# Kernel optimization log

Hardware: AMD Instinct MI355X
Metric: run time of the kernel (lower is better)

The kernel has to match this reference:

```python
import jax, jax.numpy as jnp
import numpy as np

V, D, H, B, LA, LC = 50000, 300, 256, 32, 256, 256


def setup_inputs():
    key = jax.random.key(0)
    ks = jax.random.split(key, 20)
    u = lambda k, sh, sc: jax.random.uniform(k, sh, jnp.float32, -sc, sc)
    s = 1.0 / float(np.sqrt(H))
    return {
        "anchor_input": jax.random.randint(ks[0], (B, LA), 0, V),
        "anchor_length": jax.random.randint(ks[1], (B,), 1, LA + 1),
        "candidate_input": jax.random.randint(ks[2], (B, LC), 0, V),
        "candidate_length": jax.random.randint(ks[3], (B,), 1, LC + 1),
        "batch_size": B,
        "emb": jax.random.normal(ks[4], (V, D), jnp.float32) * 0.1,
        "W_ih_a": u(ks[5], (3 * H, D), s),
        "W_hh_a": u(ks[6], (3 * H, H), s),
        "b_ih_a": u(ks[7], (3 * H,), s),
        "b_hh_a": u(ks[8], (3 * H,), s),
        "W_ih_c": u(ks[9], (3 * H, D + H), s),
        "W_hh_c": u(ks[10], (3 * H, H), s),
        "b_ih_c": u(ks[11], (3 * H,), s),
        "b_hh_c": u(ks[12], (3 * H,), s),
        "Wq": u(ks[13], (H, H), s),
        "Wk": u(ks[14], (H, H), s),
        "v_att": u(ks[15], (H,), s),
    }


def _gru_step(x, h, W_ih, W_hh, b_ih, b_hh):
    # torch GRUCell convention (gate order r, z, n)
    gi = x @ W_ih.T + b_ih
    gh = h @ W_hh.T + b_hh
    ir, iz, inn = jnp.split(gi, 3, axis=-1)
    hr, hz, hn = jnp.split(gh, 3, axis=-1)
    r = jax.nn.sigmoid(ir + hr)
    z = jax.nn.sigmoid(iz + hz)
    n = jnp.tanh(inn + r * hn)
    return (1.0 - z) * n + z * h


def _forward(anchor_input, anchor_length, candidate_input, candidate_length,
             emb, W_ih_a, W_hh_a, b_ih_a, b_hh_a,
             W_ih_c, W_hh_c, b_ih_c, b_hh_c, Wq, Wk, v_att):
    Bb = anchor_input.shape[0]
    # ---- anchor encoder: GRU with packed-sequence semantics (zero pad outputs, freeze hidden) ----
    ax = emb[anchor_input].transpose(1, 0, 2)  # [LA, B, D]
    ts_a = jnp.arange(ax.shape[0])

    def a_step(h, inp):
        xt, t = inp
        hn = _gru_step(xt, h, W_ih_a, W_hh_a, b_ih_a, b_hh_a)
        valid = (t < anchor_length)[:, None]
        h = jnp.where(valid, hn, h)
        return h, jnp.where(valid, hn, 0.0)

    h0 = jnp.zeros((Bb, H), ax.dtype)
    anchor_hidden, a_outs = jax.lax.scan(a_step, h0, (ax, ts_a))  # a_outs: [LA, B, H]
    anchor_outputs = a_outs.transpose(1, 0, 2)  # [B, LA, H]
    anchor_emb = a_outs.sum(0) / anchor_length.astype(ax.dtype)[:, None]  # meanVector

    # ---- candidate decoder: per-step additive attention + GRU + length-mask blend ----
    keys = anchor_outputs @ Wk  # [B, LA, H], precomputed once
    cx = emb[candidate_input].transpose(1, 0, 2)  # [LC, B, D]
    ts_c = jnp.arange(cx.shape[0])

    def c_step(h, inp):
        xt, t = inp
        q = h @ Wq  # [B, H] query from previous hidden
        scores = jnp.einsum('blh,h->bl', jnp.tanh(keys + q[:, None, :]), v_att)
        attn = jax.nn.softmax(scores, axis=-1)
        context = jnp.einsum('bl,blh->bh', attn, anchor_outputs)
        hn = _gru_step(jnp.concatenate([xt, context], axis=-1), h,
                       W_ih_c, W_hh_c, b_ih_c, b_hh_c)
        mask = (candidate_length < t).astype(h.dtype)[:, None]  # strict '<' is faithful to source
        h = hn * (1.0 - mask) + mask * h
        return h, h * (1.0 - mask)

    _, c_outs = jax.lax.scan(c_step, anchor_hidden, (cx, ts_c))  # [LC, B, H]
    valid_c = (ts_c[:, None] < candidate_length[None, :]).astype(cx.dtype)[:, :, None]
    candidate_emb = (c_outs * valid_c).sum(0) / candidate_length.astype(cx.dtype)[:, None]
    return anchor_emb, candidate_emb


def reference(anchor_input, anchor_length, candidate_input, candidate_length, batch_size,
              emb, W_ih_a, W_hh_a, b_ih_a, b_hh_a,
              W_ih_c, W_hh_c, b_ih_c, b_hh_c, Wq, Wk, v_att):
    return _forward(anchor_input, anchor_length, candidate_input, candidate_length,
                    emb, W_ih_a, W_hh_a, b_ih_a, b_hh_a,
                    W_ih_c, W_hh_c, b_ih_c, b_hh_c, Wq, Wk, v_att)
```

## Files before the change

### kernel.cpp

```cpp
#include <hip/hip_runtime.h>
#include <hip/hip_fp16.h>
#include <math.h>

#define BB 32
#define LAV 256
#define LCV 256
#define DV 300
#define HV 256
#define G3 768

typedef _Float16 f16x2 __attribute__((ext_vector_type(2)));
union F4H8 { float4 f4; f16x2 h2[4]; };
union U2H4 { uint2 u2; f16x2 h2[2]; };

static __device__ __forceinline__ float rcp_(float x) { return __builtin_amdgcn_rcpf(x); }
static __device__ __forceinline__ float sigm(float x) { return rcp_(1.f + __expf(-x)); }
static __device__ __forceinline__ float tanh_(float x) { return 1.f - 2.f * rcp_(1.f + __expf(2.f * x)); }

__global__ void prep_pack(const float* __restrict__ W_ih_a, const float* __restrict__ W_ih_c,
                          const float* __restrict__ W_hh_a, const float* __restrict__ W_hh_c,
                          const float* __restrict__ Wq,
                          float* __restrict__ WT_a, float* __restrict__ WT_cx,
                          __half* __restrict__ WhaRH, __half* __restrict__ WhaSH,
                          __half* __restrict__ WqH, __half* __restrict__ WrzH,
                          __half* __restrict__ WnH)
{
    int i = blockIdx.x * 256 + threadIdx.x;
    switch (blockIdx.y) {
    case 0: if (i < 230400) { int k = i / 768, n = i % 768; WT_a[i] = W_ih_a[n * 300 + k]; } break;
    case 1: if (i < 230400) { int k = i / 768, n = i % 768; WT_cx[i] = W_ih_c[n * 556 + k]; } break;
    case 2: if (i < 98304) { int e = i & 1, r = i >> 1, ii = r & 63, j = r >> 6;
            WhaRH[i] = __float2half(W_hh_a[j * 256 + 2 * ii + e]); } break;
    case 3: if (i < 98304) { int e = i & 1, s = (i >> 1) & 1, r = i >> 2, j = r % 768, i2 = r / 768;
            int k = 2 * (64 + 2 * i2 + s) + e;
            WhaSH[i] = __float2half(W_hh_a[j * 256 + k]); } break;
    case 4: if (i < 65536) { int e = i & 1, r2 = i >> 1, m = r2 & 255, k2 = r2 >> 8;
            WqH[i] = __float2half(Wq[(2 * k2 + e) * 256 + m]); } break;
    case 5: if (i < 262144) { int e = i & 1, r2 = i >> 1, j = r2 & 511, kk = r2 >> 9;
            int kh = kk >> 7, k2i = kk & 127, k = kh * 256 + 2 * k2i + e;
            float v = (k < 256) ? W_hh_c[j * 256 + k] : W_ih_c[j * 556 + 300 + (k - 256)];
            WrzH[i] = __float2half(v); } break;
    case 6: if (i < 131072) { int e = i & 1, r2 = i >> 1, j = r2 & 255, gg = r2 >> 8;
            int slot = gg >> 6, k2i = gg & 63, grp = slot >> 1, kh = slot & 1;
            int kl = kh * 128 + 2 * k2i + e;
            float v = grp ? W_ih_c[(512 + j) * 556 + 300 + kl] : W_hh_c[(512 + j) * 256 + kl];
            WnH[i] = __float2half(v); } break;
    }
}

template <int MODE>
__global__ __launch_bounds__(256) void gemm_tile(
    const float* __restrict__ X, const int* __restrict__ gidx, int ldx,
    const float* __restrict__ Wt, int K, int Nn,
    const float* __restrict__ bias, float* __restrict__ Cout)
{
    __shared__ __align__(16) float As[32][68];
    __shared__ __align__(16) float Bs[32][68];
    __shared__ int toks[64];
    int tid = threadIdx.x;
    int m0 = blockIdx.x * 64, n0 = blockIdx.y * 64;
    if (tid < 64) {
        int m = m0 + tid;
        if (gidx) { int t = m >> 5, b = m & 31; toks[tid] = gidx[b * LAV + t]; }
        else toks[tid] = m;
    }
    __syncthreads();
    float acc[4][4] = {};
    int tx = tid & 15, ty = tid >> 4;
    for (int k0 = 0; k0 < K; k0 += 32) {
        {
            int r = tid >> 2, cc = (tid & 3) * 8;
            const float* src = X + (size_t)toks[r] * ldx + k0 + cc;
            float4 v0 = {0.f,0.f,0.f,0.f}, v1 = {0.f,0.f,0.f,0.f};
            if (k0 + cc + 3 < K) v0 = *(const float4*)src;
            if (k0 + cc + 7 < K) v1 = *(const float4*)(src + 4);
            As[cc+0][r]=v0.x; As[cc+1][r]=v0.y; As[cc+2][r]=v0.z; As[cc+3][r]=v0.w;
            As[cc+4][r]=v1.x; As[cc+5][r]=v1.y; As[cc+6][r]=v1.z; As[cc+7][r]=v1.w;
        }
        {
            int kr = tid >> 4, c4 = (tid & 15) * 4;
            #pragma unroll
            for (int p = 0; p < 2; ++p) {
                float4 v = {0.f,0.f,0.f,0.f};
                int kg = k0 + kr + p * 16;
                if (kg < K) v = *(const float4*)(Wt + (size_t)kg * Nn + n0 + c4);
                *(float4*)&Bs[kr + p * 16][c4] = v;
            }
        }
        __syncthreads();
        #pragma unroll 8
        for (int kk = 0; kk < 32; ++kk) {
            float4 a4 = *(const float4*)&As[kk][ty * 4];
            float4 b4 = *(const float4*)&Bs[kk][tx * 4];
            acc[0][0]=fmaf(a4.x,b4.x,acc[0][0]); acc[0][1]=fmaf(a4.x,b4.y,acc[0][1]);
            acc[0][2]=fmaf(a4.x,b4.z,acc[0][2]); acc[0][3]=fmaf(a4.x,b4.w,acc[0][3]);
            acc[1][0]=fmaf(a4.y,b4.x,acc[1][0]); acc[1][1]=fmaf(a4.y,b4.y,acc[1][1]);
            acc[1][2]=fmaf(a4.y,b4.z,acc[1][2]); acc[1][3]=fmaf(a4.y,b4.w,acc[1][3]);
            acc[2][0]=fmaf(a4.z,b4.x,acc[2][0]); acc[2][1]=fmaf(a4.z,b4.y,acc[2][1]);
            acc[2][2]=fmaf(a4.z,b4.z,acc[2][2]); acc[2][3]=fmaf(a4.z,b4.w,acc[2][3]);
            acc[3][0]=fmaf(a4.w,b4.x,acc[3][0]); acc[3][1]=fmaf(a4.w,b4.y,acc[3][1]);
            acc[3][2]=fmaf(a4.w,b4.z,acc[3][2]); acc[3][3]=fmaf(a4.w,b4.w,acc[3][3]);
        }
        __syncthreads();
    }
    if (MODE == 0) {
        float4 bz = *(const float4*)&bias[n0 + tx * 4];
        #pragma unroll
        for (int i = 0; i < 4; ++i) {
            int m = m0 + ty * 4 + i;
            float4 o = { acc[i][0] + bz.x, acc[i][1] + bz.y, acc[i][2] + bz.z, acc[i][3] + bz.w };
            *(float4*)&Cout[(size_t)m * Nn + n0 + tx * 4] = o;
        }
    } else {
        int b_ = m0 >> 8;
        int l0 = (m0 & 255) + ty * 4;
        f16x2* TH = (f16x2*)Cout;
        #pragma unroll
        for (int j = 0; j < 4; ++j) {
            int h = n0 + tx * 4 + j;
            size_t base = ((size_t)(b_ * 256 + h)) * 128 + (l0 >> 1);
            f16x2 v01 = { (_Float16)tanh_(acc[0][j]), (_Float16)tanh_(acc[1][j]) };
            f16x2 v23 = { (_Float16)tanh_(acc[2][j]), (_Float16)tanh_(acc[3][j]) };
            TH[base] = v01;
            TH[base + 1] = v23;
        }
    }
}

__global__ __launch_bounds__(768) void anchor_rnn(
    const float* __restrict__ GI, const int* __restrict__ lens,
    const float* __restrict__ bhh, const __half* __restrict__ WhaRH,
    const __half* __restrict__ WhaSH,
    float* __restrict__ AO, __half* __restrict__ AOH,
    float* __restrict__ hid, float* __restrict__ outp)
{
    __shared__ float gh[768];
    __shared__ __align__(16) float hs[256];
    __shared__ __align__(16) f16x2 hx2[128];
    __shared__ float bhhS[768];
    int bid = blockIdx.x, tid = threadIdx.x;
    int len = lens[bid];

    f16x2 wreg[64];
    {
        const float4* s = (const float4*)WhaRH + (size_t)tid * 16;
        #pragma unroll
        for (int u = 0; u < 16; ++u) {
            F4H8 c; c.f4 = s[u];
            wreg[4*u+0] = c.h2[0]; wreg[4*u+1] = c.h2[1];
            wreg[4*u+2] = c.h2[2]; wreg[4*u+3] = c.h2[3];
        }
    }
    if (tid < 256) hs[tid] = 0.f;
    if (tid < 128) { f16x2 z = {(_Float16)0.f, (_Float16)0.f}; hx2[tid] = z; }
    bhhS[tid] = bhh[tid];
    float sum = 0.f;
    __syncthreads();

    for (int t = 0; t < LAV; ++t) {
        {
            float a0=0.f,a1=0.f,a2=0.f,a3=0.f;
            const float4* xb = (const float4*)hx2;
            #pragma unroll
            for (int u = 0; u < 16; ++u) {
                F4H8 xv; xv.f4 = xb[u];
                a0 = __builtin_amdgcn_fdot2(wreg[4*u+0], xv.h2[0], a0, false);
                a1 = __builtin_amdgcn_fdot2(wreg[4*u+1], xv.h2[1], a1, false);
                a2 = __builtin_amdgcn_fdot2(wreg[4*u+2], xv.h2[2], a2, false);
                a3 = __builtin_amdgcn_fdot2(wreg[4*u+3], xv.h2[3], a3, false);
            }
            const uint2* wsp = (const uint2*)WhaSH + tid;
            float b0=0.f,b1=0.f;
            #pragma unroll
            for (int i2 = 0; i2 < 32; ++i2) {
                U2H4 w; w.u2 = wsp[(size_t)i2 * 768];
                U2H4 xx; xx.u2 = *(const uint2*)&hx2[64 + 2 * i2];
                b0 = __builtin_amdgcn_fdot2(w.h2[0], xx.h2[0], b0, false);
                b1 = __builtin_amdgcn_fdot2(w.h2[1], xx.h2[1], b1, false);
            }
            gh[tid] = ((a0 + a1) + (a2 + a3)) + (b0 + b1) + bhhS[tid];
        }
        __syncthreads();
        if (tid < 256) {
            const float* gi = GI + ((size_t)t * BB + bid) * G3;
            float r = sigm(gi[tid] + gh[tid]);
            float z = sigm(gi[256 + tid] + gh[256 + tid]);
            float n = tanh_(fmaf(r, gh[512 + tid], gi[512 + tid]));
            float hk = hs[tid];
            float hn = (1.f - z) * n + z * hk;
            bool valid = (t < len);
            float hnew = valid ? hn : hk;
            hs[tid] = hnew;
            float ov = valid ? hn : 0.f;
            AO[((size_t)bid * LAV + t) * HV + tid] = ov;
            AOH[((size_t)bid * LAV + t) * HV + tid] = __float2half(ov);
            sum += ov;
            float other = __shfl_xor(hnew, 1, 64);
            if (!(tid & 1)) {
                f16x2 v = { (_Float16)hnew, (_Float16)other };
                hx2[tid >> 1] = v;
            }
        }
        __syncthreads();
    }
    if (tid < 256) {
        outp[bid * HV + tid] = sum / (float)len;
        hid[bid * HV + tid] = hs[tid];
    }
}

__global__ __launch_bounds__(1024) void cand_rnn(
    const float* __restrict__ GI, const int* __restrict__ lens,
    const float* __restrict__ bhh, const __half* __restrict__ WrzH,
    const __half* __restrict__ WnH, const __half* __restrict__ WqH,
    const float* __restrict__ v_att, const __half* __restrict__ AOH,
    const __half* __restrict__ TH, const float* __restrict__ hid,
    float* __restrict__ outp)
{
    __shared__ __align__(16) f16x2 x2[256];
    __shared__ __align__(16) float hs[256];
    __shared__ float tqs[256];
    __shared__ float vls[256];
    __shared__ float attn[256];
    __shared__ __align__(16) float red[3072];
    __shared__ float bhhS[768];
    __shared__ float wred[8];

    int tid = threadIdx.x;
    int b = blockIdx.x;
    int len = lens[b];

    const f16x2* Wq2  = (const f16x2*)WqH;
    const f16x2* Wrz2 = (const f16x2*)WrzH;
    const f16x2* Wn2  = (const f16x2*)WnH;
    const f16x2* T2   = (const f16x2*)TH + (size_t)b * 256 * 128;
    const f16x2* AO2  = (const f16x2*)AOH + (size_t)b * 256 * 128;

    if (tid < 256) { hs[tid] = hid[b * HV + tid]; vls[tid] = v_att[tid]; }
    if (tid < 768) bhhS[tid] = bhh[tid];
    __syncthreads();
    if (tid < 128) {
        f16x2 v = { (_Float16)hs[2 * tid], (_Float16)hs[2 * tid + 1] };
        x2[tid] = v;
    }
    __syncthreads();

    float csum = 0.f;

    for (int t = 0; t < LCV; ++t) {
        {
            int m = tid & 255, kc = tid >> 8;
            float a0 = 0.f, a1 = 0.f;
            #pragma unroll 8
            for (int i = 0; i < 32; i += 2) {
                int k2 = kc * 32 + i;
                a0 = __builtin_amdgcn_fdot2(Wq2[k2 * 256 + m], x2[k2], a0, false);
                a1 = __builtin_amdgcn_fdot2(Wq2[(k2 + 1) * 256 + m], x2[k2 + 1], a1, false);
            }
            red[kc * 256 + m] = a0 + a1;
        }
        __syncthreads();
        if (tid < 256) {
            float q = red[tid] + red[256 + tid] + red[512 + tid] + red[768 + tid];
            tqs[tid] = tanh_(q);
        }
        __syncthreads();
        {
            int l2 = tid & 127, hg = tid >> 7;
            float s0 = 0.f, s1 = 0.f;
            #pragma unroll 8
            for (int i = 0; i < 32; ++i) {
                int h = hg * 32 + i;
                f16x2 Tv = T2[(size_t)h * 128 + l2];
                float tq = tqs[h], vv = vls[h];
                float T0 = (float)Tv.x, T1 = (float)Tv.y;
                float d0 = fmaxf(fmaf(T0, tq, 1.f), 1e-6f);
                float d1 = fmaxf(fmaf(T1, tq, 1.f), 1e-6f);
                s0 = fmaf(vv * (T0 + tq), rcp_(d0), s0);
                s1 = fmaf(vv * (T1 + tq), rcp_(d1), s1);
            }
            red[hg * 256 + 2 * l2] = s0;
            red[hg * 256 + 2 * l2 + 1] = s1;
        }
        __syncthreads();
        float sv = 0.f;
        if (tid < 256) {
            #pragma unroll
            for (int hg = 0; hg < 8; ++hg) sv += red[hg * 256 + tid];
            float m = sv;
            #pragma unroll
            for (int o = 1; o < 64; o <<= 1) m = fmaxf(m, __shfl_xor(m, o, 64));
            if ((tid & 63) == 0) wred[tid >> 6] = m;
        }
        __syncthreads();
        if (tid < 256) {
            float mx = fmaxf(fmaxf(wred[0], wred[1]), fmaxf(wred[2], wred[3]));
            float e = __expf(sv - mx);
            attn[tid] = e;
            float s = e;
            #pragma unroll
            for (int o = 1; o < 64; o <<= 1) s += __shfl_xor(s, o, 64);
            if ((tid & 63) == 0) wred[4 + (tid >> 6)] = s;
        }
        __syncthreads();
        {
            int ho2 = tid & 127, lc = tid >> 7;
            float c0 = 0.f, c1 = 0.f;
            #pragma unroll 8
            for (int i = 0; i < 32; ++i) {
                int l = lc * 32 + i;
                f16x2 ao = AO2[(size_t)l * 128 + ho2];
                float w = attn[l];
                c0 = fmaf(w, (float)ao.x, c0);
                c1 = fmaf(w, (float)ao.y, c1);
            }
            red[lc * 256 + 2 * ho2] = c0;
            red[lc * 256 + 2 * ho2 + 1] = c1;
        }
        __syncthreads();
        if (tid < 128) {
            float c0 = 0.f, c1 = 0.f;
            #pragma unroll
            for (int lc = 0; lc < 8; ++lc) {
                c0 += red[lc * 256 + 2 * tid];
                c1 += red[lc * 256 + 2 * tid + 1];
            }
            float rs = rcp_(wred[4] + wred[5] + wred[6] + wred[7]);
            f16x2 v = { (_Float16)(c0 * rs), (_Float16)(c1 * rs) };
            x2[128 + tid] = v;
        }
        __syncthreads();
        {
            int j = tid & 511, kh = tid >> 9;
            float a0 = 0.f, a1 = 0.f;
            #pragma unroll 8
            for (int i = 0; i < 128; i += 2) {
                int kk = kh * 128 + i;
                a0 = __builtin_amdgcn_fdot2(Wrz2[(size_t)kk * 512 + j], x2[kk], a0, false);
                a1 = __builtin_amdgcn_fdot2(Wrz2[(size_t)(kk + 1) * 512 + j], x2[kk + 1], a1, false);
            }
            red[tid] = a0 + a1;
        }
        {
            int j = tid & 255, slot = tid >> 8;
            int grp = slot >> 1, kh = slot & 1;
            int xb = grp * 128 + kh * 64;
            float a0 = 0.f, a1 = 0.f;
            #pragma unroll 8
            for (int i = 0; i < 64; i += 2) {
                int gg = slot * 64 + i;
                a0 = __builtin_amdgcn_fdot2(Wn2[(size_t)gg * 256 + j], x2[xb + i], a0, false);
                a1 = __builtin_amdgcn_fdot2(Wn2[(size_t)(gg + 1) * 256 + j], x2[xb + i + 1], a1, false);
            }
            red[1024 + tid] = a0 + a1;
        }
        __syncthreads();
        if (tid < 256) {
            const float* gi = GI + ((size_t)t * BB + b) * G3;
            float rr = red[tid] + red[512 + tid];
            float zz = red[256 + tid] + red[768 + tid];
            float nh = red[1024 + tid] + red[1280 + tid];
            float nc = red[1536 + tid] + red[1792 + tid];
            float r = sigm(gi[tid] + rr + bhhS[tid]);
            float z = sigm(gi[256 + tid] + zz + bhhS[256 + tid]);
            float n = tanh_(gi[512 + tid] + nc + r * (nh + bhhS[512 + tid]));
            float hk = hs[tid];
            float hn = (1.f - z) * n + z * hk;
            float hnew = (len < t) ? hk : hn;
            hs[tid] = hnew;
            if (t < len) csum += hnew;
            float other = __shfl_xor(hnew, 1, 64);
            if ((tid & 1) == 0) {
                f16x2 v = { (_Float16)hnew, (_Float16)other };
                x2[tid >> 1] = v;
            }
        }
        __syncthreads();
    }
    if (tid < 256) outp[8192 + b * HV + tid] = csum / (float)len;
}

extern "C" void kernel_launch(void* const* d_in, const int* in_sizes, int n_in,
                              void* d_out, int out_size, void* d_ws, size_t ws_size,
                              hipStream_t stream) {
    const int* anchor_input     = (const int*)d_in[0];
    const int* anchor_length    = (const int*)d_in[1];
    const int* candidate_input  = (const int*)d_in[2];
    const int* candidate_length = (const int*)d_in[3];
    const float* emb    = (const float*)d_in[5];
    const float* W_ih_a = (const float*)d_in[6];
    const float* W_hh_a = (const float*)d_in[7];
    const float* b_ih_a = (const float*)d_in[8];
    const float* b_hh_a = (const float*)d_in[9];
    const float* W_ih_c = (const float*)d_in[10];
    const float* W_hh_c = (const float*)d_in[11];
    const float* b_ih_c = (const float*)d_in[12];
    const float* b_hh_c = (const float*)d_in[13];
    const float* Wq     = (const float*)d_in[14];
    const float* Wk     = (const float*)d_in[15];
    const float* v_att  = (const float*)d_in[16];
    float* out = (float*)d_out;

    float* ws = (float*)d_ws;
    size_t off = 0;
    float* GI_a  = ws + off; off += (size_t)LAV * BB * G3;
    float* GI_c  = ws + off; off += (size_t)LCV * BB * G3;
    float* AO    = ws + off; off += (size_t)BB * LAV * HV;
    float* hid   = ws + off; off += (size_t)BB * HV;
    float* WT_a  = ws + off; off += 300 * 768;
    float* WT_cx = ws + off; off += 300 * 768;
    __half* TH    = (__half*)(ws + off); off += (size_t)BB * HV * LAV / 2;
    __half* AOH   = (__half*)(ws + off); off += (size_t)BB * LAV * HV / 2;
    __half* WhaRH = (__half*)(ws + off); off += 98304 / 2;
    __half* WhaSH = (__half*)(ws + off); off += 98304 / 2;
    __half* WqH   = (__half*)(ws + off); off += 65536 / 2;
    __half* WrzH  = (__half*)(ws + off); off += 262144 / 2;
    __half* WnH   = (__half*)(ws + off); off += 131072 / 2;

    prep_pack<<<dim3(1024, 7), 256, 0, stream>>>(W_ih_a, W_ih_c, W_hh_a, W_hh_c, Wq,
                                                 WT_a, WT_cx, WhaRH, WhaSH, WqH, WrzH, WnH);
    gemm_tile<0><<<dim3(128, 12), 256, 0, stream>>>(emb, anchor_input, DV, WT_a, DV, G3, b_ih_a, GI_a);
    gemm_tile<0><<<dim3(128, 12), 256, 0, stream>>>(emb, candidate_input, DV, WT_cx, DV, G3, b_ih_c, GI_c);
    anchor_rnn<<<32, 768, 0, stream>>>(GI_a, anchor_length, b_hh_a, WhaRH, WhaSH, AO, AOH, hid, out);
    gemm_tile<1><<<dim3(128, 4), 256, 0, stream>>>(AO, nullptr, HV, Wk, HV, HV, nullptr, (float*)TH);
    cand_rnn<<<32, 1024, 0, stream>>>(GI_c, candidate_length, b_hh_c, WrzH, WnH, WqH,
                                      v_att, AOH, TH, hid, out);
}
```

Before: 4.218 ms.

## Hoist hidden-state GRU matvecs earlier and drop softmax max reduction

```diff
diff --git a/kernel.cpp b/kernel.cpp
--- a/kernel.cpp
+++ b/kernel.cpp
@@ -222,7 +222,9 @@
     __shared__ float tqs[256];
     __shared__ float vls[256];
     __shared__ float attn[256];
-    __shared__ __align__(16) float red[3072];
+    __shared__ __align__(16) float redBig[2048];
+    __shared__ __align__(16) float redRZh[1024];
+    __shared__ __align__(16) float redNh[1024];
     __shared__ float bhhS[768];
     __shared__ float wred[8];
 
@@ -257,11 +259,33 @@
                 a0 = __builtin_amdgcn_fdot2(Wq2[k2 * 256 + m], x2[k2], a0, false);
                 a1 = __builtin_amdgcn_fdot2(Wq2[(k2 + 1) * 256 + m], x2[k2 + 1], a1, false);
             }
-            red[kc * 256 + m] = a0 + a1;
+            redBig[kc * 256 + m] = a0 + a1;
+        }
+        {
+            int j = tid & 511, kh2 = tid >> 9;
+            float a0 = 0.f, a1 = 0.f;
+            #pragma unroll 8
+            for (int i = 0; i < 64; i += 2) {
+                int kk = kh2 * 64 + i;
+                a0 = __builtin_amdgcn_fdot2(Wrz2[(size_t)kk * 512 + j], x2[kk], a0, false);
+                a1 = __builtin_amdgcn_fdot2(Wrz2[(size_t)(kk + 1) * 512 + j], x2[kk + 1], a1, false);
+            }
+            redRZh[tid] = a0 + a1;
+        }
+        {
+            int j = tid & 255, q4 = tid >> 8;
+            float a0 = 0.f, a1 = 0.f;
+            #pragma unroll 8
+            for (int i = 0; i < 32; i += 2) {
+                int gg = q4 * 32 + i;
+                a0 = __builtin_amdgcn_fdot2(Wn2[(size_t)gg * 256 + j], x2[gg], a0, false);
+                a1 = __builtin_amdgcn_fdot2(Wn2[(size_t)(gg + 1) * 256 + j], x2[gg + 1], a1, false);
+            }
+            redNh[tid] = a0 + a1;
         }
         __syncthreads();
         if (tid < 256) {
-            float q = red[tid] + red[256 + tid] + red[512 + tid] + red[768 + tid];
+            float q = redBig[tid] + redBig[256 + tid] + redBig[512 + tid] + redBig[768 + tid];
             tqs[tid] = tanh_(q);
         }
         __syncthreads();
@@ -279,23 +303,15 @@
                 s0 = fmaf(vv * (T0 + tq), rcp_(d0), s0);
                 s1 = fmaf(vv * (T1 + tq), rcp_(d1), s1);
             }
-            red[hg * 256 + 2 * l2] = s0;
-            red[hg * 256 + 2 * l2 + 1] = s1;
-        }
-        __syncthreads();
-        float sv = 0.f;
+            redBig[hg * 256 + 2 * l2] = s0;
+            redBig[hg * 256 + 2 * l2 + 1] = s1;
+        }
+        __syncthreads();
         if (tid < 256) {
-            #pragma unroll
-            for (int hg = 0; hg < 8; ++hg) sv += red[hg * 256 + tid];
-            float m = sv;
-            #pragma unroll
-            for (int o = 1; o < 64; o <<= 1) m = fmaxf(m, __shfl_xor(m, o, 64));
-            if ((tid & 63) == 0) wred[tid >> 6] = m;
-        }
-        __syncthreads();
-        if (tid < 256) {
-            float mx = fmaxf(fmaxf(wred[0], wred[1]), fmaxf(wred[2], wred[3]));
-            float e = __expf(sv - mx);
+            float sv = 0.f;
+            #pragma unroll
+            for (int hg = 0; hg < 8; ++hg) sv += redBig[hg * 256 + tid];
+            float e = __expf(sv);
             attn[tid] = e;
             float s = e;
             #pragma unroll
@@ -314,16 +330,16 @@
                 c0 = fmaf(w, (float)ao.x, c0);
                 c1 = fmaf(w, (float)ao.y, c1);
             }
-            red[lc * 256 + 2 * ho2] = c0;
-            red[lc * 256 + 2 * ho2 + 1] = c1;
+            redBig[lc * 256 + 2 * ho2] = c0;
+            redBig[lc * 256 + 2 * ho2 + 1] = c1;
         }
         __syncthreads();
         if (tid < 128) {
             float c0 = 0.f, c1 = 0.f;
             #pragma unroll
             for (int lc = 0; lc < 8; ++lc) {
-                c0 += red[lc * 256 + 2 * tid];
-                c1 += red[lc * 256 + 2 * tid + 1];
+                c0 += redBig[lc * 256 + 2 * tid];
+                c1 += redBig[lc * 256 + 2 * tid + 1];
             }
             float rs = rcp_(wred[4] + wred[5] + wred[6] + wred[7]);
             f16x2 v = { (_Float16)(c0 * rs), (_Float16)(c1 * rs) };
@@ -331,36 +347,34 @@
         }
         __syncthreads();
         {
-            int j = tid & 511, kh = tid >> 9;
+            int j = tid & 511, kh2 = tid >> 9;
             float a0 = 0.f, a1 = 0.f;
             #pragma unroll 8
-            for (int i = 0; i < 128; i += 2) {
-                int kk = kh * 128 + i;
+            for (int i = 0; i < 64; i += 2) {
+                int kk = 128 + kh2 * 64 + i;
                 a0 = __builtin_amdgcn_fdot2(Wrz2[(size_t)kk * 512 + j], x2[kk], a0, false);
                 a1 = __builtin_amdgcn_fdot2(Wrz2[(size_t)(kk + 1) * 512 + j], x2[kk + 1], a1, false);
             }
-            red[tid] = a0 + a1;
-        }
-        {
-            int j = tid & 255, slot = tid >> 8;
-            int grp = slot >> 1, kh = slot & 1;
-            int xb = grp * 128 + kh * 64;
+            redBig[tid] = a0 + a1;
+        }
+        {
+            int j = tid & 255, q4 = tid >> 8;
             float a0 = 0.f, a1 = 0.f;
             #pragma unroll 8
-            for (int i = 0; i < 64; i += 2) {
-                int gg = slot * 64 + i;
-                a0 = __builtin_amdgcn_fdot2(Wn2[(size_t)gg * 256 + j], x2[xb + i], a0, false);
-                a1 = __builtin_amdgcn_fdot2(Wn2[(size_t)(gg + 1) * 256 + j], x2[xb + i + 1], a1, false);
-            }
-            red[1024 + tid] = a0 + a1;
+            for (int i = 0; i < 32; i += 2) {
+                int gg = 128 + q4 * 32 + i;
+                a0 = __builtin_amdgcn_fdot2(Wn2[(size_t)gg * 256 + j], x2[gg], a0, false);
+                a1 = __builtin_amdgcn_fdot2(Wn2[(size_t)(gg + 1) * 256 + j], x2[gg + 1], a1, false);
+            }
+            redBig[1024 + tid] = a0 + a1;
         }
         __syncthreads();
         if (tid < 256) {
             const float* gi = GI + ((size_t)t * BB + b) * G3;
-            float rr = red[tid] + red[512 + tid];
-            float zz = red[256 + tid] + red[768 + tid];
-            float nh = red[1024 + tid] + red[1280 + tid];
-            float nc = red[1536 + tid] + red[1792 + tid];
+            float rr = (redRZh[tid] + redRZh[512 + tid]) + (redBig[tid] + redBig[512 + tid]);
+            float zz = (redRZh[256 + tid] + redRZh[768 + tid]) + (redBig[256 + tid] + redBig[768 + tid]);
+            float nh = (redNh[tid] + redNh[256 + tid]) + (redNh[512 + tid] + redNh[768 + tid]);
+            float nc = (redBig[1024 + tid] + redBig[1280 + tid]) + (redBig[1536 + tid] + redBig[1792 + tid]);
             float r = sigm(gi[tid] + rr + bhhS[tid]);
             float z = sigm(gi[256 + tid] + zz + bhhS[256 + tid]);
             float n = tanh_(gi[512 + tid] + nc + r * (nh + bhhS[512 + tid]));
```

Result: faster. 3.837 ms (-9.0%).
